# Performance work log

Hardware: AMD Instinct MI355X
Metric: run time of the kernel (lower is better)

## Reference

```python
import jax, jax.numpy as jnp
import numpy as np

B, L, D, E, K, DFF = 2, 2048, 1024, 8, 2, 4096


def setup_inputs() -> dict:
    key = jax.random.key(0)
    kx, kr, kg, ku, kd = jax.random.split(key, 5)
    scale = 0.02
    return {
        "x": jax.random.normal(kx, (B, L, D), dtype=jnp.float32),
        "Wr": jax.random.normal(kr, (E, D), dtype=jnp.float32) * scale,   # router: logits = x @ Wr.T
        "Wg": jax.random.normal(kg, (E, DFF, D), dtype=jnp.float32) * scale,  # gate proj per expert
        "Wu": jax.random.normal(ku, (E, DFF, D), dtype=jnp.float32) * scale,  # up proj per expert
        "Wd": jax.random.normal(kd, (E, D, DFF), dtype=jnp.float32) * scale,  # down proj per expert
    }


def reference(x, Wr, Wg, Wu, Wd):
    Bb, Ll, Dd = x.shape
    T = Bb * Ll
    xt = x.reshape(T, Dd)                                   # [T, D]
    logits = jnp.einsum("td,ed->te", xt, Wr)                # router logits [T, E]
    scores = jax.nn.softmax(logits, axis=-1)
    k_scores, k_ids = jax.lax.top_k(scores, K)              # [T, K]
    eps = jnp.finfo(x.dtype).eps
    k_w = k_scores / (k_scores.sum(axis=-1, keepdims=True) + eps)  # renormalized top-k weights
    # combine[t, e] = sum_k k_w[t, k] * (k_ids[t, k] == e)
    combine = jnp.sum(jax.nn.one_hot(k_ids, E, dtype=x.dtype) * k_w[..., None], axis=1)  # [T, E]
    # GluMLP per expert, computed densely over all tokens (reference form)
    g = jnp.einsum("td,efd->etf", xt, Wg)                   # [E, T, DFF]
    u = jnp.einsum("td,efd->etf", xt, Wu)                   # [E, T, DFF]
    h = jax.nn.relu(g) * u
    out_e = jnp.einsum("etf,edf->etd", h, Wd)               # [E, T, D]
    out = jnp.einsum("te,etd->td", combine, out_e)          # weighted combine [T, D]
    return out.reshape(Bb, Ll, Dd)
```

## Files before the change

kernel.cpp:

```cpp
#include <hip/hip_runtime.h>
#include <hip/hip_bf16.h>

#define Tt 4096
#define Dd 1024
#define Ee 8
#define Kk 2
#define Ff 4096

using f32x4  = __attribute__((ext_vector_type(4))) float;
using bf16x8 = __attribute__((ext_vector_type(8))) short;

__device__ __forceinline__ unsigned short f2bf(float f) {
    union { float fp; unsigned int u; } v; v.fp = f;
    unsigned int u = v.u;
    return (unsigned short)((u + 0x7FFFu + ((u >> 16) & 1u)) >> 16);
}

__device__ __forceinline__ void gl16(const void* g, void* l) {
    __builtin_amdgcn_global_load_lds(
        (const __attribute__((address_space(1))) void*)g,
        (__attribute__((address_space(3))) void*)l, 16, 0, 0);
}

__global__ void router_kernel(const float* __restrict__ x, const float* __restrict__ Wr,
                              int* __restrict__ ids, float* __restrict__ wts,
                              int* __restrict__ counts, unsigned short* __restrict__ xb) {
    const int t = blockIdx.x;
    const int lane = threadIdx.x;
    const float* xr = x + (size_t)t * Dd + lane * 16;
    float xv[16];
#pragma unroll
    for (int i = 0; i < 4; ++i) *(float4*)(xv + 4 * i) = *(const float4*)(xr + 4 * i);
    uint4 o0, o1;
    o0.x = (unsigned)f2bf(xv[0])  | ((unsigned)f2bf(xv[1])  << 16);
    o0.y = (unsigned)f2bf(xv[2])  | ((unsigned)f2bf(xv[3])  << 16);
    o0.z = (unsigned)f2bf(xv[4])  | ((unsigned)f2bf(xv[5])  << 16);
    o0.w = (unsigned)f2bf(xv[6])  | ((unsigned)f2bf(xv[7])  << 16);
    o1.x = (unsigned)f2bf(xv[8])  | ((unsigned)f2bf(xv[9])  << 16);
    o1.y = (unsigned)f2bf(xv[10]) | ((unsigned)f2bf(xv[11]) << 16);
    o1.z = (unsigned)f2bf(xv[12]) | ((unsigned)f2bf(xv[13]) << 16);
    o1.w = (unsigned)f2bf(xv[14]) | ((unsigned)f2bf(xv[15]) << 16);
    unsigned short* xo = xb + (size_t)t * Dd + lane * 16;
    *(uint4*)(xo) = o0;
    *(uint4*)(xo + 8) = o1;

    double dot[Ee];
#pragma unroll
    for (int e = 0; e < Ee; ++e) {
        const float* wr = Wr + e * Dd + lane * 16;
        double s = 0.0;
#pragma unroll
        for (int i = 0; i < 16; ++i) s += (double)xv[i] * (double)wr[i];
        dot[e] = s;
    }
#pragma unroll
    for (int off = 32; off >= 1; off >>= 1) {
#pragma unroll
        for (int e = 0; e < Ee; ++e) dot[e] += __shfl_xor(dot[e], off, 64);
    }
    if (lane == 0) {
        float lg[Ee];
#pragma unroll
        for (int e = 0; e < Ee; ++e) lg[e] = (float)dot[e];
        float m = lg[0];
        for (int e = 1; e < Ee; ++e) m = fmaxf(m, lg[e]);
        float ex[Ee]; float sum = 0.f;
        for (int e = 0; e < Ee; ++e) { ex[e] = expf(lg[e] - m); sum += ex[e]; }
        float s0 = -1.f, s1 = -1.f; int i0 = 0, i1 = 0;
        for (int e = 0; e < Ee; ++e) {
            float s = ex[e];
            if (s > s0)      { s1 = s0; i1 = i0; s0 = s; i0 = e; }
            else if (s > s1) { s1 = s; i1 = e; }
        }
        float inv = 1.f / sum;
        float sc0 = s0 * inv, sc1 = s1 * inv;
        float den = sc0 + sc1 + 1.1920929e-7f;
        ids[2 * t] = i0; ids[2 * t + 1] = i1;
        wts[2 * t] = sc0 / den; wts[2 * t + 1] = sc1 / den;
        atomicAdd(&counts[i0], 1);
        atomicAdd(&counts[i1], 1);
    }
}

__global__ void cvtw_kernel(const float* __restrict__ src, unsigned short* __restrict__ dst) {
    size_t i = ((size_t)blockIdx.x * blockDim.x + threadIdx.x) * 8;
    float4 a = *(const float4*)(src + i);
    float4 b = *(const float4*)(src + i + 4);
    uint4 o;
    o.x = (unsigned)f2bf(a.x) | ((unsigned)f2bf(a.y) << 16);
    o.y = (unsigned)f2bf(a.z) | ((unsigned)f2bf(a.w) << 16);
    o.z = (unsigned)f2bf(b.x) | ((unsigned)f2bf(b.y) << 16);
    o.w = (unsigned)f2bf(b.z) | ((unsigned)f2bf(b.w) << 16);
    *(uint4*)(dst + i) = o;
}

__global__ void cvt_wgu_kernel(const float* __restrict__ Wg, const float* __restrict__ Wu,
                               unsigned short* __restrict__ Wgu) {
    size_t tid = (size_t)blockIdx.x * blockDim.x + threadIdx.x;
    size_t row = tid >> 7;
    int dc  = (int)(tid & 127);
    int e   = (int)(row >> 13);
    int j   = (int)(row & 8191);
    int fg = j >> 5, s = (j >> 4) & 1, fi = j & 15;
    int f  = fg * 16 + fi;
    const float* src = (s ? Wu : Wg) + ((size_t)e * Ff + f) * Dd + dc * 8;
    float4 a = *(const float4*)(src);
    float4 b = *(const float4*)(src + 4);
    uint4 o;
    o.x = (unsigned)f2bf(a.x) | ((unsigned)f2bf(a.y) << 16);
    o.y = (unsigned)f2bf(a.z) | ((unsigned)f2bf(a.w) << 16);
    o.z = (unsigned)f2bf(b.x) | ((unsigned)f2bf(b.y) << 16);
    o.w = (unsigned)f2bf(b.z) | ((unsigned)f2bf(b.w) << 16);
    *(uint4*)(Wgu + row * Dd + dc * 8) = o;
}

__global__ void scan_kernel(const int* __restrict__ counts, int* __restrict__ cursor,
                            int* __restrict__ eoff) {
    if (threadIdx.x == 0) {
        int acc = 0;
        for (int e = 0; e < Ee; ++e) { eoff[e] = acc; cursor[e] = acc; acc += counts[e]; }
        eoff[Ee] = acc;
    }
}

__global__ void scatter_kernel(const int* __restrict__ ids,
                               int* __restrict__ cursor, int* __restrict__ rows) {
    int t = blockIdx.x * blockDim.x + threadIdx.x;
    if (t >= Tt) return;
#pragma unroll
    for (int k = 0; k < Kk; ++k) {
        int e = ids[2 * t + k];
        int pos = atomicAdd(&cursor[e], 1);
        rows[pos] = 2 * t + k;
    }
}


#define MFMA_BF16(a, b, c) __builtin_amdgcn_mfma_f32_16x16x32_bf16(a, b, c, 0, 0, 0)

template<bool G2>
__launch_bounds__(512, 1)
__global__ void gemm_8ph(const unsigned short* __restrict__ Abase,
                         const unsigned short* __restrict__ Bbase,
                         const int* __restrict__ eoff, const int* __restrict__ rows,
                         unsigned short* __restrict__ H,
                         float* __restrict__ partial) {
    constexpr int KLEN = G2 ? Ff : Dd;
    constexpr int NT   = (G2 ? 2048 : 1024) / 64;
    const int e   = blockIdx.z;
    const int off = eoff[e];
    const int ne  = eoff[e + 1] - off;
    const int my  = G2 ? (blockIdx.y >> 1) : blockIdx.y;
    const int sK  = G2 ? (blockIdx.y & 1) : 0;
    const int koff = sK * 2048;
    const int m0  = my * 256;
    if (m0 >= ne) return;
    const int n0  = blockIdx.x * 256;

    __shared__ __align__(16) unsigned short Ls[65536];

    const int tid  = threadIdx.x;
    const int lane = tid & 63;
    const int w    = tid >> 6;
    const int wr   = w >> 2;
    const int wc   = w & 3;
    const int lr   = lane & 15;
    const int lc   = lane >> 4;

    const int sr = lane >> 3;
    const int cA = (lane & 7) ^ sr;
    int asrc[4];
#pragma unroll
    for (int qq = 0; qq < 4; ++qq) {
        int rr = m0 + qq * 64 + w * 8 + sr;
        if (rr > ne - 1) rr = ne - 1;
        asrc[qq] = (G2 ? (off + rr) : (rows[off + rr] >> 1)) * KLEN + cA * 8;
    }
    const unsigned short* Bp = Bbase + (size_t)e * (G2 ? (size_t)Dd * Ff : (size_t)8192 * Dd);
    int bsrc[4];
#pragma unroll
    for (int qq = 0; qq < 4; ++qq) {
        int rN = n0 + qq * 64 + w * 8 + sr;
        bsrc[qq] = rN * KLEN + cA * 8;
    }

    auto STAGE_A = [&](int T, int Hh) {
        const int bo_ = (T & 1) * 32768; const int kt_ = koff + T * 64;
        gl16(Abase + asrc[2 * Hh]     + kt_, Ls + bo_ + (2 * Hh)     * 4096 + w * 512);
        gl16(Abase + asrc[2 * Hh + 1] + kt_, Ls + bo_ + (2 * Hh + 1) * 4096 + w * 512);
    };
    auto STAGE_B = [&](int T, int Hh) {
        const int bo_ = (T & 1) * 32768 + 16384; const int kt_ = koff + T * 64;
        gl16(Bp + bsrc[2 * Hh]     + kt_, Ls + bo_ + (2 * Hh)     * 4096 + w * 512);
        gl16(Bp + bsrc[2 * Hh + 1] + kt_, Ls + bo_ + (2 * Hh + 1) * 4096 + w * 512);
    };

    const int ccx0 = ((0 * 4 + lc) ^ (lr & 7)) * 8;
    const int ccx1 = ((1 * 4 + lc) ^ (lr & 7)) * 8;
    const int aB = wr * 8192 + lr * 64;
    const int bB = 16384 + wc * 4096 + lr * 64;

    f32x4 acc[8][4];
#pragma unroll
    for (int m = 0; m < 8; ++m)
#pragma unroll
        for (int n = 0; n < 4; ++n) acc[m][n] = (f32x4){0.f, 0.f, 0.f, 0.f};

    STAGE_A(0, 0); STAGE_A(0, 1); STAGE_B(0, 0); STAGE_B(0, 1);
    STAGE_A(1, 0); STAGE_A(1, 1);
    asm volatile("s_waitcnt vmcnt(4)" ::: "memory");
    __builtin_amdgcn_sched_barrier(0);
    __builtin_amdgcn_s_barrier();

    bf16x8 a0[8], a1[8], b0[4], b1[4];

    for (int t = 0; t < NT; ++t) {
        const int bo = (t & 1) * 32768;
#pragma unroll
        for (int m = 0; m < 8; ++m) a0[m] = *(const bf16x8*)(Ls + bo + aB + m * 1024 + ccx0);
#pragma unroll
        for (int n = 0; n < 4; ++n) b0[n] = *(const bf16x8*)(Ls + bo + bB + n * 1024 + ccx0);
        if (t + 1 < NT) STAGE_B(t + 1, 0);
        __builtin_amdgcn_s_barrier();
        asm volatile("s_waitcnt lgkmcnt(0)" ::: "memory");
        __builtin_amdgcn_sched_barrier(0);
        __builtin_amdgcn_s_setprio(1);
#pragma unroll
        for (int m = 0; m < 8; ++m) {
            acc[m][0] = MFMA_BF16(a0[m], b0[0], acc[m][0]);
            acc[m][1] = MFMA_BF16(a0[m], b0[1], acc[m][1]);
        }
        __builtin_amdgcn_s_setprio(0);
        __builtin_amdgcn_s_barrier();
#pragma unroll
        for (int m = 0; m < 8; ++m) a1[m] = *(const bf16x8*)(Ls + bo + aB + m * 1024 + ccx1);
        if (t + 1 < NT) STAGE_B(t + 1, 1);
        __builtin_amdgcn_s_barrier();
        __builtin_amdgcn_s_setprio(1);
#pragma unroll
        for (int m = 0; m < 8; ++m) {
            acc[m][2] = MFMA_BF16(a0[m], b0[2], acc[m][2]);
            acc[m][3] = MFMA_BF16(a0[m], b0[3], acc[m][3]);
        }
        __builtin_amdgcn_s_setprio(0);
        asm volatile("s_waitcnt lgkmcnt(0)" ::: "memory");
        __builtin_amdgcn_sched_barrier(0);
        __builtin_amdgcn_s_barrier();
#pragma unroll
        for (int n = 0; n < 4; ++n) b1[n] = *(const bf16x8*)(Ls + bo + bB + n * 1024 + ccx1);
        if (t + 2 < NT) STAGE_A(t + 2, 0);
        __builtin_amdgcn_s_barrier();
        asm volatile("s_waitcnt lgkmcnt(0)" ::: "memory");
        __builtin_amdgcn_sched_barrier(0);
        __builtin_amdgcn_s_setprio(1);
#pragma unroll
        for (int m = 0; m < 8; ++m) {
            acc[m][0] = MFMA_BF16(a1[m], b1[0], acc[m][0]);
            acc[m][1] = MFMA_BF16(a1[m], b1[1], acc[m][1]);
        }
        __builtin_amdgcn_s_setprio(0);
        __builtin_amdgcn_s_barrier();
        if (t + 2 < NT) STAGE_A(t + 2, 1);
        __builtin_amdgcn_s_setprio(1);
#pragma unroll
        for (int m = 0; m < 8; ++m) {
            acc[m][2] = MFMA_BF16(a1[m], b1[2], acc[m][2]);
            acc[m][3] = MFMA_BF16(a1[m], b1[3], acc[m][3]);
        }
        __builtin_amdgcn_s_setprio(0);
        if (t + 2 < NT) { asm volatile("s_waitcnt vmcnt(4)" ::: "memory"); }
        else            { asm volatile("s_waitcnt vmcnt(0)" ::: "memory"); }
        __builtin_amdgcn_sched_barrier(0);
        __builtin_amdgcn_s_barrier();
    }

    if constexpr (!G2) {
        const int fg16 = ((n0 + wc * 64) >> 5) * 16 + lr;
#pragma unroll
        for (int m = 0; m < 8; ++m) {
            const int itok = m0 + wr * 128 + m * 16 + (lane >> 4) * 4;
#pragma unroll
            for (int r = 0; r < 4; ++r) {
                const int i = itok + r;
                if (i < ne) {
                    unsigned short* hp = H + (size_t)(off + i) * Ff;
#pragma unroll
                    for (int np = 0; np < 2; ++np) {
                        const float g = acc[m][2 * np][r];
                        const float u = acc[m][2 * np + 1][r];
                        hp[fg16 + np * 16] = f2bf(fmaxf(g, 0.f) * u);
                    }
                }
            }
        }
    } else {
        const int dbase = n0 + wc * 64;
#pragma unroll
        for (int m = 0; m < 8; ++m) {
            const int ib = m0 + wr * 128 + m * 16 + (lane >> 4) * 4;
#pragma unroll
            for (int r = 0; r < 4; ++r) {
                const int i = ib + r;
                if (i < ne) {
                    const int tr = rows[off + i];
                    float* op = partial + ((size_t)sK * 8192 + tr) * Dd + dbase + lr;
#pragma unroll
                    for (int n = 0; n < 4; ++n) op[n * 16] = acc[m][n][r];
                }
            }
        }
    }
}

__global__ void reduce_kernel(const float* __restrict__ P, const float* __restrict__ wts,
                              float* __restrict__ out) {
    const size_t idx = (size_t)blockIdx.x * blockDim.x + threadIdx.x;
    const size_t t  = idx >> 8;
    const int   dq  = (int)(idx & 255);
    const float w0 = wts[2 * t], w1 = wts[2 * t + 1];
    const float4* p00 = (const float4*)(P + (2 * t)        * Dd) + dq;
    const float4* p01 = (const float4*)(P + (2 * t + 1)    * Dd) + dq;
    const float4* p10 = (const float4*)(P + ((size_t)8192 + 2 * t)     * Dd) + dq;
    const float4* p11 = (const float4*)(P + ((size_t)8192 + 2 * t + 1) * Dd) + dq;
    float4 a = *p00, b = *p01, c = *p10, d = *p11;
    float4 o;
    o.x = w0 * (a.x + c.x) + w1 * (b.x + d.x);
    o.y = w0 * (a.y + c.y) + w1 * (b.y + d.y);
    o.z = w0 * (a.z + c.z) + w1 * (b.z + d.z);
    o.w = w0 * (a.w + c.w) + w1 * (b.w + d.w);
    ((float4*)(out + t * Dd))[dq] = o;
}

extern "C" void kernel_launch(void* const* d_in, const int* in_sizes, int n_in,
                              void* d_out, int out_size, void* d_ws, size_t ws_size,
                              hipStream_t stream) {
    const float* x  = (const float*)d_in[0];
    const float* Wr = (const float*)d_in[1];
    const float* Wg = (const float*)d_in[2];
    const float* Wu = (const float*)d_in[3];
    const float* Wd = (const float*)d_in[4];
    float* out = (float*)d_out;
    char* ws = (char*)d_ws;

    const size_t WELEM    = (size_t)Ee * Ff * Dd;
    const size_t OFF_IDS  = 256;
    const size_t OFF_WTS  = OFF_IDS  + (size_t)Tt * 2 * 4;
    const size_t OFF_ROWS = OFF_WTS  + (size_t)Tt * 2 * 4;
    const size_t OFF_ROWW = OFF_ROWS + (size_t)Tt * Kk * 4;
    const size_t OFF_XB   = OFF_ROWW + (size_t)Tt * Kk * 4;
    const size_t OFF_H    = OFF_XB   + (size_t)Tt * Dd * 2;
    const size_t OFF_WGU  = OFF_H    + (size_t)Tt * Kk * Ff * 2;
    const size_t OFF_WD   = OFF_WGU  + WELEM * 2 * 2;
    const size_t NEED     = OFF_WD   + WELEM * 2;
    if (ws_size < NEED) return;

    int* counts = (int*)ws;
    int* cursor = (int*)(ws + 32);
    int* eoff   = (int*)(ws + 64);
    int* ids    = (int*)(ws + OFF_IDS);
    float* wts  = (float*)(ws + OFF_WTS);
    int* rows   = (int*)(ws + OFF_ROWS);
    unsigned short* xb  = (unsigned short*)(ws + OFF_XB);
    unsigned short* H   = (unsigned short*)(ws + OFF_H);
    unsigned short* Wgu = (unsigned short*)(ws + OFF_WGU);
    unsigned short* Wdb = (unsigned short*)(ws + OFF_WD);
    float* partial = (float*)(ws + OFF_WGU);

    hipMemsetAsync(ws, 0, 256, stream);

    router_kernel  <<<Tt, 64, 0, stream>>>(x, Wr, ids, wts, counts, xb);
    scan_kernel    <<<1, 64, 0, stream>>>(counts, cursor, eoff);
    scatter_kernel <<<Tt / 256, 256, 0, stream>>>(ids, cursor, rows);

    cvt_wgu_kernel <<<(int)(WELEM * 2 / 8 / 256), 256, 0, stream>>>(Wg, Wu, Wgu);
    cvtw_kernel    <<<(int)(WELEM / 8 / 256), 256, 0, stream>>>(Wd, Wdb);

    gemm_8ph<false><<<dim3(2 * Ff / 256, Tt / 256, Ee), 512, 0, stream>>>(
        xb, Wgu, eoff, rows, H, partial);
    gemm_8ph<true> <<<dim3(Dd / 256, 2 * (Tt / 256), Ee), 512, 0, stream>>>(
        H, Wdb, eoff, rows, H, partial);

    reduce_kernel  <<<(Tt * Dd / 4) / 256, 256, 0, stream>>>(partial, wts, out);
}
```

Before: 517.7 us.

## Merge weight conversion kernels, swizzle GEMM block order, drop explicit LDS waits

Combines the two fp32-to-bf16 weight conversion launches into one kernel that branches on block index, saving a launch and its tail. Remaps the GEMM workgroup index with an XCD-style swizzle so consecutive blocks land on the same chiplet and share cache for weights and activations. Removes two explicit lgkmcnt waits and sched barriers before MFMA phases, leaving LDS-read waits to the compiler. This risks scheduling changes, and the swizzle assumes the grid size divides by 8.

```diff
diff --git a/kernel.cpp b/kernel.cpp
--- a/kernel.cpp
+++ b/kernel.cpp
@@ -82,36 +82,38 @@
     }
 }
 
-__global__ void cvtw_kernel(const float* __restrict__ src, unsigned short* __restrict__ dst) {
-    size_t i = ((size_t)blockIdx.x * blockDim.x + threadIdx.x) * 8;
-    float4 a = *(const float4*)(src + i);
-    float4 b = *(const float4*)(src + i + 4);
-    uint4 o;
-    o.x = (unsigned)f2bf(a.x) | ((unsigned)f2bf(a.y) << 16);
-    o.y = (unsigned)f2bf(a.z) | ((unsigned)f2bf(a.w) << 16);
-    o.z = (unsigned)f2bf(b.x) | ((unsigned)f2bf(b.y) << 16);
-    o.w = (unsigned)f2bf(b.z) | ((unsigned)f2bf(b.w) << 16);
-    *(uint4*)(dst + i) = o;
-}
-
-__global__ void cvt_wgu_kernel(const float* __restrict__ Wg, const float* __restrict__ Wu,
-                               unsigned short* __restrict__ Wgu) {
-    size_t tid = (size_t)blockIdx.x * blockDim.x + threadIdx.x;
-    size_t row = tid >> 7;
-    int dc  = (int)(tid & 127);
-    int e   = (int)(row >> 13);
-    int j   = (int)(row & 8191);
-    int fg = j >> 5, s = (j >> 4) & 1, fi = j & 15;
-    int f  = fg * 16 + fi;
-    const float* src = (s ? Wu : Wg) + ((size_t)e * Ff + f) * Dd + dc * 8;
-    float4 a = *(const float4*)(src);
-    float4 b = *(const float4*)(src + 4);
-    uint4 o;
-    o.x = (unsigned)f2bf(a.x) | ((unsigned)f2bf(a.y) << 16);
-    o.y = (unsigned)f2bf(a.z) | ((unsigned)f2bf(a.w) << 16);
-    o.z = (unsigned)f2bf(b.x) | ((unsigned)f2bf(b.y) << 16);
-    o.w = (unsigned)f2bf(b.z) | ((unsigned)f2bf(b.w) << 16);
-    *(uint4*)(Wgu + row * Dd + dc * 8) = o;
+__global__ void cvt_all_kernel(const float* __restrict__ Wg, const float* __restrict__ Wu,
+                               const float* __restrict__ Wd,
+                               unsigned short* __restrict__ Wgu, unsigned short* __restrict__ Wdb) {
+    const int bid = blockIdx.x;
+    if (bid < 32768) {
+        size_t tid = (size_t)bid * blockDim.x + threadIdx.x;
+        size_t row = tid >> 7;
+        int dc  = (int)(tid & 127);
+        int e   = (int)(row >> 13);
+        int j   = (int)(row & 8191);
+        int fg = j >> 5, s = (j >> 4) & 1, fi = j & 15;
+        int f  = fg * 16 + fi;
+        const float* src = (s ? Wu : Wg) + ((size_t)e * Ff + f) * Dd + dc * 8;
+        float4 a = *(const float4*)(src);
+        float4 b = *(const float4*)(src + 4);
+        uint4 o;
+        o.x = (unsigned)f2bf(a.x) | ((unsigned)f2bf(a.y) << 16);
+        o.y = (unsigned)f2bf(a.z) | ((unsigned)f2bf(a.w) << 16);
+        o.z = (unsigned)f2bf(b.x) | ((unsigned)f2bf(b.y) << 16);
+        o.w = (unsigned)f2bf(b.z) | ((unsigned)f2bf(b.w) << 16);
+        *(uint4*)(Wgu + row * Dd + dc * 8) = o;
+    } else {
+        size_t i = ((size_t)(bid - 32768) * blockDim.x + threadIdx.x) * 8;
+        float4 a = *(const float4*)(Wd + i);
+        float4 b = *(const float4*)(Wd + i + 4);
+        uint4 o;
+        o.x = (unsigned)f2bf(a.x) | ((unsigned)f2bf(a.y) << 16);
+        o.y = (unsigned)f2bf(a.z) | ((unsigned)f2bf(a.w) << 16);
+        o.z = (unsigned)f2bf(b.x) | ((unsigned)f2bf(b.y) << 16);
+        o.w = (unsigned)f2bf(b.z) | ((unsigned)f2bf(b.w) << 16);
+        *(uint4*)(Wdb + i) = o;
+    }
 }
 
 __global__ void scan_kernel(const int* __restrict__ counts, int* __restrict__ cursor,
@@ -150,12 +152,19 @@
     const int e   = blockIdx.z;
     const int off = eoff[e];
     const int ne  = eoff[e + 1] - off;
-    const int my  = G2 ? (blockIdx.y >> 1) : blockIdx.y;
-    const int sK  = G2 ? (blockIdx.y & 1) : 0;
+
+    const int nwg = gridDim.x * gridDim.y;
+    const int f_  = blockIdx.x + gridDim.x * blockIdx.y;
+    const int swz = (f_ & 7) * (nwg >> 3) + (f_ >> 3);
+    const int bx  = swz % gridDim.x;
+    const int by  = swz / gridDim.x;
+
+    const int my  = G2 ? (by >> 1) : by;
+    const int sK  = G2 ? (by & 1) : 0;
     const int koff = sK * 2048;
     const int m0  = my * 256;
     if (m0 >= ne) return;
-    const int n0  = blockIdx.x * 256;
+    const int n0  = bx * 256;
 
     __shared__ __align__(16) unsigned short Ls[65536];
 
@@ -222,8 +231,6 @@
         for (int n = 0; n < 4; ++n) b0[n] = *(const bf16x8*)(Ls + bo + bB + n * 1024 + ccx0);
         if (t + 1 < NT) STAGE_B(t + 1, 0);
         __builtin_amdgcn_s_barrier();
-        asm volatile("s_waitcnt lgkmcnt(0)" ::: "memory");
-        __builtin_amdgcn_sched_barrier(0);
         __builtin_amdgcn_s_setprio(1);
 #pragma unroll
         for (int m = 0; m < 8; ++m) {
@@ -250,8 +257,6 @@
         for (int n = 0; n < 4; ++n) b1[n] = *(const bf16x8*)(Ls + bo + bB + n * 1024 + ccx1);
         if (t + 2 < NT) STAGE_A(t + 2, 0);
         __builtin_amdgcn_s_barrier();
-        asm volatile("s_waitcnt lgkmcnt(0)" ::: "memory");
-        __builtin_amdgcn_sched_barrier(0);
         __builtin_amdgcn_s_setprio(1);
 #pragma unroll
         for (int m = 0; m < 8; ++m) {
@@ -372,8 +377,7 @@
     scan_kernel    <<<1, 64, 0, stream>>>(counts, cursor, eoff);
     scatter_kernel <<<Tt / 256, 256, 0, stream>>>(ids, cursor, rows);
 
-    cvt_wgu_kernel <<<(int)(WELEM * 2 / 8 / 256), 256, 0, stream>>>(Wg, Wu, Wgu);
-    cvtw_kernel    <<<(int)(WELEM / 8 / 256), 256, 0, stream>>>(Wd, Wdb);
+    cvt_all_kernel <<<49152, 256, 0, stream>>>(Wg, Wu, Wd, Wgu, Wdb);
 
     gemm_8ph<false><<<dim3(2 * Ff / 256, Tt / 256, Ee), 512, 0, stream>>>(
         xb, Wgu, eoff, rows, H, partial);
```

Measured after the change: 929.7 us. 79.6% more time.
